# Performance work log

Hardware: AMD Instinct MI355X
Metric: run time of the kernel (lower is better)

## Reference

```python
import jax, jax.numpy as jnp
import numpy as np

B, D, HID, DC, K = 32768, 64, 512, 128, 12
CLAMP = 1.0
L1 = D // 2          # GLOW split lengths
L2 = D - L1
INIT = 0.01          # torch code rescales all params to 0.01*randn


def setup_inputs() -> dict:
    key = jax.random.key(0)
    ks = iter(jax.random.split(key, 16))
    # FrEIA PermuteRandom: np.random.seed(k); np.random.permutation(D)
    perms = jnp.asarray(
        np.stack([np.random.RandomState(k).permutation(D) for k in range(K)]),
        dtype=jnp.int32)
    f32 = jnp.float32
    return {
        'q_feat': jax.random.normal(next(ks), (B, 1, D), f32),
        'H': jax.random.normal(next(ks), (B, DC), f32),
        'perms': perms,
        'an_logscale': INIT * jax.random.normal(next(ks), (K, D), f32),
        'an_bias': INIT * jax.random.normal(next(ks), (K, D), f32),
        's1_W1': INIT * jax.random.normal(next(ks), (K, HID, L1 + DC), f32),
        's1_b1': INIT * jax.random.normal(next(ks), (K, HID), f32),
        's1_W2': INIT * jax.random.normal(next(ks), (K, 2 * L2, HID), f32),
        's1_b2': INIT * jax.random.normal(next(ks), (K, 2 * L2), f32),
        's2_W1': INIT * jax.random.normal(next(ks), (K, HID, L2 + DC), f32),
        's2_b1': INIT * jax.random.normal(next(ks), (K, HID), f32),
        's2_W2': INIT * jax.random.normal(next(ks), (K, 2 * L1, HID), f32),
        's2_b2': INIT * jax.random.normal(next(ks), (K, 2 * L1), f32),
    }


def _mlp(x, W1, b1, W2, b2):
    # torch Linear: y = x @ W.T + b
    h = jax.nn.relu(x @ W1.T + b1)
    return h @ W2.T + b2


def _log_e(s):
    # FrEIA GLOW soft clamp: log e(s) = clamp * 0.636 * atan(s / clamp)
    return CLAMP * 0.636 * jnp.arctan(s / CLAMP)


def reference(q_feat, H, perms, an_logscale, an_bias,
              s1_W1, s1_b1, s1_W2, s1_b2,
              s2_W1, s2_b1, s2_W2, s2_b2):
    x = q_feat.reshape(q_feat.shape[0], -1)          # Flatten: (B,1,D)->(B,D)
    logj = jnp.zeros(x.shape[0], x.dtype)

    def block(carry, p):
        x, logj = carry
        perm, ls, bi, w11, b11, w12, b12, w21, b21, w22, b22 = p
        x = x[:, perm]                               # PermuteRandom (logdet 0)
        x = x * jnp.exp(ls) + bi                     # ActNorm
        logj = logj + jnp.sum(ls)
        x1, x2 = x[:, :L1], x[:, L1:]                # GLOW coupling
        r2 = _mlp(jnp.concatenate([x2, H], 1), w21, b21, w22, b22)
        le2 = _log_e(r2[:, :L1])
        y1 = jnp.exp(le2) * x1 + r2[:, L1:]
        r1 = _mlp(jnp.concatenate([y1, H], 1), w11, b11, w12, b12)
        le1 = _log_e(r1[:, :L2])
        y2 = jnp.exp(le1) * x2 + r1[:, L2:]
        logj = logj + jnp.sum(le1, axis=1) + jnp.sum(le2, axis=1)
        return (jnp.concatenate([y1, y2], 1), logj), None

    (z, logj), _ = jax.lax.scan(
        block, (x, logj),
        (perms, an_logscale, an_bias,
         s1_W1, s1_b1, s1_W2, s1_b2,
         s2_W1, s2_b1, s2_W2, s2_b2))
    return z, logj
```

## Files before the change

kernel.cpp:

```cpp
#include <hip/hip_runtime.h>
#include <hip/hip_bf16.h>
#include <math.h>

#define B_ROWS 32768

typedef __attribute__((ext_vector_type(8)))  short        s8v;
typedef __attribute__((ext_vector_type(4)))  float        f4v;
typedef __attribute__((ext_vector_type(2)))  unsigned int u2v;
typedef __attribute__((ext_vector_type(4)))  unsigned int u4v;

__device__ __forceinline__ short f2bf(float f){
  unsigned u = __builtin_bit_cast(unsigned, f);
  u = (u + 0x7fffu + ((u >> 16) & 1u)) >> 16;
  return (short)u;
}
__device__ __forceinline__ unsigned pk2(float a, float b){
  return (unsigned)(unsigned short)f2bf(a) | ((unsigned)(unsigned short)f2bf(b) << 16);
}
__device__ __forceinline__ float bf_lo(unsigned u){ return __builtin_bit_cast(float, u << 16); }
__device__ __forceinline__ float bf_hi(unsigned u){ return __builtin_bit_cast(float, u & 0xffff0000u); }

#define MFMA16(A,B,C) __builtin_amdgcn_mfma_f32_16x16x32_bf16((A),(B),(C),0,0,0)

#define OXFT 0
#define XFT_S 132
#define OHB  33792
#define HB_S 136
#define OW1  68608
#define W1BUF 43008
#define W1_S 168
#define OB1  154624
#define OB2  158720
#define OLJ  159232
#define OPERM 159744
#define OELS 160000
#define OBIV 160256
#define OSLS 160512
#define SM_SZ 160528

#define SL_S 68
#define SLOT_B 17408

#define O_S1W1 0
#define O_S1W2 983040
#define O_S2W1 1376256
#define O_S2W2 2359296
#define W_TOTAL 2752512

__global__ void cvtw(const float* __restrict__ s1w1, const float* __restrict__ s1w2,
                     const float* __restrict__ s2w1, const float* __restrict__ s2w2,
                     unsigned short* __restrict__ dst)
{
  long t = (long)blockIdx.x * blockDim.x + threadIdx.x;
  if (t >= W_TOTAL) return;
  float v;
  if      (t < O_S1W2) v = s1w1[t];
  else if (t < O_S2W1) v = s1w2[t - O_S1W2];
  else if (t < O_S2W2) v = s2w1[t - O_S2W1];
  else                 v = s2w2[t - O_S2W2];
  dst[t] = (unsigned short)f2bf(v);
}

template<int USEBF>
__device__ __forceinline__ s8v ldw(const unsigned short* wb, const float* wf, int off){
  if (USEBF){
    return *(const s8v*)(wb + off);
  } else {
    f4v a = *(const f4v*)(wf + off);
    f4v b = *(const f4v*)(wf + off + 4);
    s8v r;
    r[0]=f2bf(a[0]); r[1]=f2bf(a[1]); r[2]=f2bf(a[2]); r[3]=f2bf(a[3]);
    r[4]=f2bf(b[0]); r[5]=f2bf(b[1]); r[6]=f2bf(b[2]); r[7]=f2bf(b[3]);
    return r;
  }
}

struct MP { const unsigned short* w1b; const float* w1f;
            const unsigned short* w2b; const float* w2f;
            const float* b1; const float* b2; };

__device__ __forceinline__ MP getmp(int m, const unsigned short* wbf,
    const float* s1W1f, const float* s1W2f, const float* s2W1f, const float* s2W2f,
    const float* s1b1, const float* s1b2, const float* s2b1, const float* s2b2)
{
  int blk = m >> 1;
  MP r;
  if (m & 1){
    r.w1b = wbf + O_S1W1 + (size_t)blk*81920; r.w1f = s1W1f + (size_t)blk*81920;
    r.w2b = wbf + O_S1W2 + (size_t)blk*32768; r.w2f = s1W2f + (size_t)blk*32768;
    r.b1 = s1b1 + blk*512; r.b2 = s1b2 + blk*64;
  } else {
    r.w1b = wbf + O_S2W1 + (size_t)blk*81920; r.w1f = s2W1f + (size_t)blk*81920;
    r.w2b = wbf + O_S2W2 + (size_t)blk*32768; r.w2f = s2W2f + (size_t)blk*32768;
    r.b1 = s2b1 + blk*512; r.b2 = s2b2 + blk*64;
  }
  return r;
}

template<int USEBF>
__device__ __forceinline__ void issue_w1(const MP& p, int cchunk, int tid,
                                         u4v wt[5], f4v wtf[10])
{
  if (USEBF){
    const unsigned short* s = p.w1b + cchunk*20480;
    #pragma unroll
    for (int k = 0; k < 5; ++k) wt[k] = *(const u4v*)(s + (size_t)(k*512+tid)*8);
  } else {
    const float* s = p.w1f + cchunk*20480;
    #pragma unroll
    for (int k = 0; k < 10; ++k) wtf[k] = *(const f4v*)(s + (size_t)(k*512+tid)*4);
  }
}

template<int USEBF>
__device__ __forceinline__ void write_w1(char* sm, int buf, int tid,
                                         const u4v wt[5], const f4v wtf[10])
{
  short* W1n = (short*)(sm + OW1 + buf*W1BUF);
  if (USEBF){
    #pragma unroll
    for (int k = 0; k < 5; ++k){
      int i = k*512 + tid, row = i/20, c16 = i - row*20;
      *(u4v*)(W1n + row*W1_S + c16*8) = wt[k];
    }
  } else {
    #pragma unroll
    for (int k = 0; k < 10; ++k){
      int i = k*512 + tid, row = i/40, c4 = i - row*40;
      f4v v = wtf[k];
      *(u2v*)(W1n + row*W1_S + c4*4) = (u2v){pk2(v[0],v[1]), pk2(v[2],v[3])};
    }
  }
}

template<int USEBF>
__device__ __forceinline__ void load_w2(const MP& p, int c, int hw, int l15, int lq, s8v w2o[4]){
  #pragma unroll
  for (int ot = 0; ot < 4; ++ot)
    w2o[ot] = ldw<USEBF>(p.w2b, p.w2f, (ot*16 + l15)*512 + c*128 + hw*32 + lq*8);
}

template<int USEBF>
__device__ __forceinline__ void mlp_body(char* sm, int tid, int m,
    const MP& cur, const MP& nxt, const s8v hfr[4][4], s8v w2cur[4])
{
  const int lane = tid & 63, wave = tid >> 6;
  const int hw = wave >> 1, ng = wave & 1;
  const int l15 = lane & 15, lq = lane >> 4;
  const int bp = m & 1;
  float* XFT = (float*)(sm + OXFT);
  short* HB  = (short*)(sm + OHB);
  float* B1L = (float*)(sm + OB1);
  float* B2L = (float*)(sm + OB2);
  float* LOGJ= (float*)(sm + OLJ);

  const int xbase = bp ? 0 : 32;
  s8v xk[4];
  #pragma unroll
  for (int nt = 0; nt < 4; ++nt){
    int b = ng*64 + nt*16 + l15;
    s8v v;
    #pragma unroll
    for (int i = 0; i < 8; ++i)
      v[i] = f2bf(XFT[(xbase + lq*8 + i)*XFT_S + b]);
    xk[nt] = v;
  }

  f4v racc[4][4];
  #pragma unroll
  for (int ot = 0; ot < 4; ++ot){
    f4v bv = (f4v){0.f,0.f,0.f,0.f};
    if (hw == 0) bv = *(const f4v*)(B2L + bp*64 + ot*16 + lq*4);
    #pragma unroll
    for (int nt = 0; nt < 4; ++nt) racc[ot][nt] = bv;
  }

  #pragma unroll
  for (int c = 0; c < 4; ++c){
    u4v wt[5]; f4v wtf[10];
    const MP& pn = (c < 3) ? cur : nxt;
    const int cn = (c < 3) ? c + 1 : 0;
    issue_w1<USEBF>(pn, cn, tid, wt, wtf);
    float b1t = 0.f, b2t = 0.f;
    if (c == 3){
      b1t = nxt.b1[tid];
      if (tid < 64) b2t = nxt.b2[tid];
    }

    const short* W1c = (const short*)(sm + OW1 + (c&1)*W1BUF);
    f4v acc[2][4];
    #pragma unroll
    for (int mt = 0; mt < 2; ++mt){
      f4v bv = *(const f4v*)(B1L + bp*512 + c*128 + hw*32 + mt*16 + lq*4);
      #pragma unroll
      for (int nt = 0; nt < 4; ++nt) acc[mt][nt] = bv;
    }
    #pragma unroll
    for (int kk = 0; kk < 5; ++kk){
      s8v a0 = *(const s8v*)(W1c + (hw*32 +  0 + l15)*W1_S + kk*32 + lq*8);
      s8v a1 = *(const s8v*)(W1c + (hw*32 + 16 + l15)*W1_S + kk*32 + lq*8);
      #pragma unroll
      for (int nt = 0; nt < 4; ++nt){
        s8v bb = (kk == 0) ? xk[nt] : hfr[nt][kk-1];
        acc[0][nt] = MFMA16(a0, bb, acc[0][nt]);
        acc[1][nt] = MFMA16(a1, bb, acc[1][nt]);
      }
    }
    #pragma unroll
    for (int mt = 0; mt < 2; ++mt)
      #pragma unroll
      for (int nt = 0; nt < 4; ++nt){
        float h0 = fmaxf(acc[mt][nt][0],0.f), h1 = fmaxf(acc[mt][nt][1],0.f);
        float h2 = fmaxf(acc[mt][nt][2],0.f), h3 = fmaxf(acc[mt][nt][3],0.f);
        *(u2v*)(HB + (ng*64 + nt*16 + l15)*HB_S + hw*32 + mt*16 + lq*4) = (u2v){pk2(h0,h1), pk2(h2,h3)};
      }
    #pragma unroll
    for (int nt = 0; nt < 4; ++nt){
      s8v bb = *(const s8v*)(HB + (ng*64 + nt*16 + l15)*HB_S + hw*32 + lq*8);
      #pragma unroll
      for (int ot = 0; ot < 4; ++ot)
        racc[ot][nt] = MFMA16(w2cur[ot], bb, racc[ot][nt]);
    }
    write_w1<USEBF>(sm, cn & 1, tid, wt, wtf);
    if (c == 3){
      B1L[(bp^1)*512 + tid] = b1t;
      if (tid < 64) B2L[(bp^1)*64 + tid] = b2t;
    }
    load_w2<USEBF>(pn, cn, hw, l15, lq, w2cur);
    __syncthreads();
  }

  {
    short* SL = (hw < 2) ? (short*)(sm + OW1 + W1BUF + hw*SLOT_B)
                         : (short*)(sm + OHB + (hw-2)*SLOT_B);
    #pragma unroll
    for (int ot = 0; ot < 4; ++ot)
      #pragma unroll
      for (int nt = 0; nt < 4; ++nt)
        *(u2v*)(SL + (ng*64 + nt*16 + l15)*SL_S + ot*16 + lq*4) =
          (u2v){pk2(racc[ot][nt][0], racc[ot][nt][1]), pk2(racc[ot][nt][2], racc[ot][nt][3])};
  }
  __syncthreads();

  {
    int b = tid & 127, og = tid >> 7;
    float le[8] = {0,0,0,0,0,0,0,0}, ra[8] = {0,0,0,0,0,0,0,0};
    #pragma unroll
    for (int mslot = 0; mslot < 4; ++mslot){
      const short* SL = (mslot < 2) ? (const short*)(sm + OW1 + W1BUF + mslot*SLOT_B)
                                    : (const short*)(sm + OHB + (mslot-2)*SLOT_B);
      u2v L0 = *(const u2v*)(SL + b*SL_S + og*8);
      u2v L1 = *(const u2v*)(SL + b*SL_S + og*8 + 4);
      u2v R0 = *(const u2v*)(SL + b*SL_S + 32 + og*8);
      u2v R1 = *(const u2v*)(SL + b*SL_S + 32 + og*8 + 4);
      le[0]+=bf_lo(L0[0]); le[1]+=bf_hi(L0[0]); le[2]+=bf_lo(L0[1]); le[3]+=bf_hi(L0[1]);
      le[4]+=bf_lo(L1[0]); le[5]+=bf_hi(L1[0]); le[6]+=bf_lo(L1[1]); le[7]+=bf_hi(L1[1]);
      ra[0]+=bf_lo(R0[0]); ra[1]+=bf_hi(R0[0]); ra[2]+=bf_lo(R0[1]); ra[3]+=bf_hi(R0[1]);
      ra[4]+=bf_lo(R1[0]); ra[5]+=bf_hi(R1[0]); ra[6]+=bf_lo(R1[1]); ra[7]+=bf_hi(R1[1]);
    }
    float part = 0.f;
    #pragma unroll
    for (int j = 0; j < 8; ++j){
      float l = 0.636f * atanf(le[j]);
      int d = bp*32 + og*8 + j;
      float y = __expf(l) * XFT[d*XFT_S + b] + ra[j];
      XFT[d*XFT_S + b] = y;
      part += l;
    }
    atomicAdd(&LOGJ[b], part);
  }
  __syncthreads();
}

template<int USEBF>
__global__ __launch_bounds__(512, 2) void cinn_t(
    const float* __restrict__ q, const float* __restrict__ Hg,
    const int* __restrict__ perms,
    const float* __restrict__ ls_g, const float* __restrict__ bi_g,
    const float* __restrict__ s1b1, const float* __restrict__ s1b2,
    const float* __restrict__ s2b1, const float* __restrict__ s2b2,
    const unsigned short* __restrict__ wbf,
    const float* __restrict__ s1W1f, const float* __restrict__ s1W2f,
    const float* __restrict__ s2W1f, const float* __restrict__ s2W2f,
    float* __restrict__ outz, float* __restrict__ outlj)
{
  __shared__ __align__(16) char sm[SM_SZ];
  const int tid = threadIdx.x;
  const int rowbase = blockIdx.x * 128;
  const int lane = tid & 63, wave = tid >> 6;
  const int hw = wave >> 1, ng = wave & 1;
  const int l15 = lane & 15, lq = lane >> 4;

  float* XFT = (float*)(sm + OXFT);
  float* B1L = (float*)(sm + OB1);
  float* B2L = (float*)(sm + OB2);
  float* LOGJ = (float*)(sm + OLJ);
  int*   PERM = (int*)(sm + OPERM);
  float* ELS  = (float*)(sm + OELS);
  float* BIV  = (float*)(sm + OBIV);
  float* SLSp = (float*)(sm + OSLS);

  {
    int b = tid >> 2, j = tid & 3;
    const float* src = q + (size_t)(rowbase + b)*64 + j*16;
    #pragma unroll
    for (int i = 0; i < 4; ++i){
      f4v v = *(const f4v*)(src + 4*i);
      #pragma unroll
      for (int jj = 0; jj < 4; ++jj)
        XFT[(j*16 + 4*i + jj)*XFT_S + b] = v[jj];
    }
  }
  if (tid < 128) LOGJ[tid] = 0.f;
  if (tid == 0)  *SLSp = 0.f;
  __syncthreads();
  if (tid < 64){
    float p = 0.f;
    #pragma unroll
    for (int k = 0; k < 12; ++k) p += ls_g[k*64 + tid];
    atomicAdd(SLSp, p);
  }

  s8v hfr[4][4];
  #pragma unroll
  for (int nt = 0; nt < 4; ++nt){
    int b = rowbase + ng*64 + nt*16 + l15;
    #pragma unroll
    for (int kkh = 0; kkh < 4; ++kkh){
      const float* hp = Hg + (size_t)b*128 + kkh*32 + lq*8;
      f4v a = *(const f4v*)hp;
      f4v c = *(const f4v*)(hp + 4);
      s8v r;
      r[0]=f2bf(a[0]); r[1]=f2bf(a[1]); r[2]=f2bf(a[2]); r[3]=f2bf(a[3]);
      r[4]=f2bf(c[0]); r[5]=f2bf(c[1]); r[6]=f2bf(c[2]); r[7]=f2bf(c[3]);
      hfr[nt][kkh] = r;
    }
  }

  s8v w2cur[4];
  {
    MP p0 = getmp(0, wbf, s1W1f, s1W2f, s2W1f, s2W2f, s1b1, s1b2, s2b1, s2b2);
    u4v wt[5]; f4v wtf[10];
    issue_w1<USEBF>(p0, 0, tid, wt, wtf);
    write_w1<USEBF>(sm, 0, tid, wt, wtf);
    B1L[tid] = p0.b1[tid];
    if (tid < 64) B2L[tid] = p0.b2[tid];
    load_w2<USEBF>(p0, 0, hw, l15, lq, w2cur);
  }

  for (int m = 0; m < 24; ++m){
    if (!(m & 1)){
      int blk = m >> 1;
      if (tid < 64){
        PERM[tid] = perms[blk*64 + tid];
        ELS[tid]  = __expf(ls_g[blk*64 + tid]);
        BIV[tid]  = bi_g[blk*64 + tid];
      }
      __syncthreads();
      {
        int d = lane, bg = wave;
        int pd = PERM[d];
        f4v v[4];
        #pragma unroll
        for (int i = 0; i < 4; ++i)
          v[i] = *(const f4v*)(XFT + pd*XFT_S + bg*16 + 4*i);
        __syncthreads();
        float e = ELS[d], bi = BIV[d];
        #pragma unroll
        for (int i = 0; i < 4; ++i){
          #pragma unroll
          for (int jj = 0; jj < 4; ++jj) v[i][jj] = fmaf(v[i][jj], e, bi);
          *(f4v*)(XFT + d*XFT_S + bg*16 + 4*i) = v[i];
        }
      }
      __syncthreads();
    }
    MP cur = getmp(m, wbf, s1W1f, s1W2f, s2W1f, s2W2f, s1b1, s1b2, s2b1, s2b2);
    MP nxt = getmp(m < 23 ? m + 1 : 23, wbf, s1W1f, s1W2f, s2W1f, s2W2f, s1b1, s1b2, s2b1, s2b2);
    mlp_body<USEBF>(sm, tid, m, cur, nxt, hfr, w2cur);
  }

  {
    int b = tid >> 2, j = tid & 3;
    float* dst = outz + (size_t)(rowbase + b)*64 + j*16;
    #pragma unroll
    for (int i = 0; i < 4; ++i){
      f4v w;
      #pragma unroll
      for (int jj = 0; jj < 4; ++jj)
        w[jj] = XFT[(j*16 + 4*i + jj)*XFT_S + b];
      *(f4v*)(dst + 4*i) = w;
    }
  }
  if (tid < 128) outlj[rowbase + tid] = LOGJ[tid] + *SLSp;
}

extern "C" void kernel_launch(void* const* d_in, const int* in_sizes, int n_in,
                              void* d_out, int out_size, void* d_ws, size_t ws_size,
                              hipStream_t stream)
{
  const float* q    = (const float*)d_in[0];
  const float* Hg   = (const float*)d_in[1];
  const int*   perms= (const int*)  d_in[2];
  const float* ls   = (const float*)d_in[3];
  const float* bi   = (const float*)d_in[4];
  const float* s1W1 = (const float*)d_in[5];
  const float* s1b1 = (const float*)d_in[6];
  const float* s1W2 = (const float*)d_in[7];
  const float* s1b2 = (const float*)d_in[8];
  const float* s2W1 = (const float*)d_in[9];
  const float* s2b1 = (const float*)d_in[10];
  const float* s2W2 = (const float*)d_in[11];
  const float* s2b2 = (const float*)d_in[12];
  float* outz  = (float*)d_out;
  float* outlj = outz + (size_t)B_ROWS * 64;

  int usebf = (ws_size >= (size_t)W_TOTAL * 2) ? 1 : 0;
  unsigned short* wbf = (unsigned short*)d_ws;
  if (usebf){
    cvtw<<<2688, 1024, 0, stream>>>(s1W1, s1W2, s2W1, s2W2, wbf);
    cinn_t<1><<<256, 512, 0, stream>>>(q, Hg, perms, ls, bi,
                                       s1b1, s1b2, s2b1, s2b2,
                                       wbf, s1W1, s1W2, s2W1, s2W2,
                                       outz, outlj);
  } else {
    cinn_t<0><<<256, 512, 0, stream>>>(q, Hg, perms, ls, bi,
                                       s1b1, s1b2, s2b1, s2b2,
                                       wbf, s1W1, s1W2, s2W1, s2W2,
                                       outz, outlj);
  }
}
```

Before: 299.2 us.

## Keep biases in registers, precompute W1 store indices, use hardware bf16 packing

Biases for both MLP layers now live in per-thread registers, loaded from global memory one chunk ahead, so the shared-memory bias buffers and their stores are removed. The per-thread row and column indices for the W1 staging stores are computed once instead of being recomputed by integer division every chunk. Float-to-bf16 conversion switches to the library __float2bfloat16 with paired packing. Launch bounds drop from 2 blocks per CU to 1, which frees registers for the extra state but may cost occupancy.

```diff
diff --git a/kernel.cpp b/kernel.cpp
--- a/kernel.cpp
+++ b/kernel.cpp
@@ -14,8 +14,10 @@
   u = (u + 0x7fffu + ((u >> 16) & 1u)) >> 16;
   return (short)u;
 }
-__device__ __forceinline__ unsigned pk2(float a, float b){
-  return (unsigned)(unsigned short)f2bf(a) | ((unsigned)(unsigned short)f2bf(b) << 16);
+__device__ __forceinline__ unsigned cpk(float a, float b){
+  __hip_bfloat16_raw lo = (__hip_bfloat16_raw)__float2bfloat16(a);
+  __hip_bfloat16_raw hi = (__hip_bfloat16_raw)__float2bfloat16(b);
+  return (unsigned)lo.x | ((unsigned)hi.x << 16);
 }
 __device__ __forceinline__ float bf_lo(unsigned u){ return __builtin_bit_cast(float, u << 16); }
 __device__ __forceinline__ float bf_hi(unsigned u){ return __builtin_bit_cast(float, u & 0xffff0000u); }
@@ -29,17 +31,16 @@
 #define OW1  68608
 #define W1BUF 43008
 #define W1_S 168
-#define OB1  154624
-#define OB2  158720
-#define OLJ  159232
-#define OPERM 159744
-#define OELS 160000
-#define OBIV 160256
-#define OSLS 160512
-#define SM_SZ 160528
+#define OLJ  154624
+#define OPERM 155136
+#define OELS 155392
+#define OBIV 155648
+#define OSLS 155904
+#define SM_SZ 155920
 
 #define SL_S 68
 #define SLOT_B 17408
+#define OSL0 (OW1 + W1BUF)
 
 #define O_S1W1 0
 #define O_S1W2 983040
@@ -68,10 +69,8 @@
   } else {
     f4v a = *(const f4v*)(wf + off);
     f4v b = *(const f4v*)(wf + off + 4);
-    s8v r;
-    r[0]=f2bf(a[0]); r[1]=f2bf(a[1]); r[2]=f2bf(a[2]); r[3]=f2bf(a[3]);
-    r[4]=f2bf(b[0]); r[5]=f2bf(b[1]); r[6]=f2bf(b[2]); r[7]=f2bf(b[3]);
-    return r;
+    u4v u = {cpk(a[0],a[1]), cpk(a[2],a[3]), cpk(b[0],b[1]), cpk(b[2],b[3])};
+    return __builtin_bit_cast(s8v, u);
   }
 }
 
@@ -113,22 +112,20 @@
 }
 
 template<int USEBF>
-__device__ __forceinline__ void write_w1(char* sm, int buf, int tid,
-                                         const u4v wt[5], const f4v wtf[10])
+__device__ __forceinline__ void write_w1(char* sm, int buf,
+                                         const u4v wt[5], const f4v wtf[10],
+                                         const int* wr, const int* wc)
 {
   short* W1n = (short*)(sm + OW1 + buf*W1BUF);
   if (USEBF){
     #pragma unroll
-    for (int k = 0; k < 5; ++k){
-      int i = k*512 + tid, row = i/20, c16 = i - row*20;
-      *(u4v*)(W1n + row*W1_S + c16*8) = wt[k];
-    }
+    for (int k = 0; k < 5; ++k)
+      *(u4v*)(W1n + wr[k]*W1_S + wc[k]*8) = wt[k];
   } else {
     #pragma unroll
     for (int k = 0; k < 10; ++k){
-      int i = k*512 + tid, row = i/40, c4 = i - row*40;
       f4v v = wtf[k];
-      *(u2v*)(W1n + row*W1_S + c4*4) = (u2v){pk2(v[0],v[1]), pk2(v[2],v[3])};
+      *(u2v*)(W1n + wr[k]*W1_S + wc[k]*4) = (u2v){cpk(v[0],v[1]), cpk(v[2],v[3])};
     }
   }
 }
@@ -142,7 +139,8 @@
 
 template<int USEBF>
 __device__ __forceinline__ void mlp_body(char* sm, int tid, int m,
-    const MP& cur, const MP& nxt, const s8v hfr[4][4], s8v w2cur[4])
+    const MP& cur, const MP& nxt, const s8v hfr[4][4], s8v w2cur[4],
+    f4v b1cur[2], f4v b2cur[4], const int* wr, const int* wc)
 {
   const int lane = tid & 63, wave = tid >> 6;
   const int hw = wave >> 1, ng = wave & 1;
@@ -150,8 +148,6 @@
   const int bp = m & 1;
   float* XFT = (float*)(sm + OXFT);
   short* HB  = (short*)(sm + OHB);
-  float* B1L = (float*)(sm + OB1);
-  float* B2L = (float*)(sm + OB2);
   float* LOGJ= (float*)(sm + OLJ);
 
   const int xbase = bp ? 0 : 32;
@@ -159,18 +155,19 @@
   #pragma unroll
   for (int nt = 0; nt < 4; ++nt){
     int b = ng*64 + nt*16 + l15;
-    s8v v;
-    #pragma unroll
-    for (int i = 0; i < 8; ++i)
-      v[i] = f2bf(XFT[(xbase + lq*8 + i)*XFT_S + b]);
-    xk[nt] = v;
+    const float* xp = XFT + (xbase + lq*8)*XFT_S + b;
+    u4v u;
+    #pragma unroll
+    for (int p = 0; p < 4; ++p)
+      u[p] = cpk(xp[(2*p)*XFT_S], xp[(2*p+1)*XFT_S]);
+    xk[nt] = __builtin_bit_cast(s8v, u);
   }
 
   f4v racc[4][4];
   #pragma unroll
   for (int ot = 0; ot < 4; ++ot){
     f4v bv = (f4v){0.f,0.f,0.f,0.f};
-    if (hw == 0) bv = *(const f4v*)(B2L + bp*64 + ot*16 + lq*4);
+    if (hw == 0) bv = b2cur[ot];
     #pragma unroll
     for (int nt = 0; nt < 4; ++nt) racc[ot][nt] = bv;
   }
@@ -181,17 +178,19 @@
     const MP& pn = (c < 3) ? cur : nxt;
     const int cn = (c < 3) ? c + 1 : 0;
     issue_w1<USEBF>(pn, cn, tid, wt, wtf);
-    float b1t = 0.f, b2t = 0.f;
-    if (c == 3){
-      b1t = nxt.b1[tid];
-      if (tid < 64) b2t = nxt.b2[tid];
+    f4v b1n0 = *(const f4v*)(pn.b1 + cn*128 + hw*32 + lq*4);
+    f4v b1n1 = *(const f4v*)(pn.b1 + cn*128 + hw*32 + 16 + lq*4);
+    if (c == 3 && hw == 0){
+      #pragma unroll
+      for (int ot = 0; ot < 4; ++ot)
+        b2cur[ot] = *(const f4v*)(nxt.b2 + ot*16 + lq*4);
     }
 
     const short* W1c = (const short*)(sm + OW1 + (c&1)*W1BUF);
     f4v acc[2][4];
     #pragma unroll
     for (int mt = 0; mt < 2; ++mt){
-      f4v bv = *(const f4v*)(B1L + bp*512 + c*128 + hw*32 + mt*16 + lq*4);
+      f4v bv = b1cur[mt];
       #pragma unroll
       for (int nt = 0; nt < 4; ++nt) acc[mt][nt] = bv;
     }
@@ -212,7 +211,7 @@
       for (int nt = 0; nt < 4; ++nt){
         float h0 = fmaxf(acc[mt][nt][0],0.f), h1 = fmaxf(acc[mt][nt][1],0.f);
         float h2 = fmaxf(acc[mt][nt][2],0.f), h3 = fmaxf(acc[mt][nt][3],0.f);
-        *(u2v*)(HB + (ng*64 + nt*16 + l15)*HB_S + hw*32 + mt*16 + lq*4) = (u2v){pk2(h0,h1), pk2(h2,h3)};
+        *(u2v*)(HB + (ng*64 + nt*16 + l15)*HB_S + hw*32 + mt*16 + lq*4) = (u2v){cpk(h0,h1), cpk(h2,h3)};
       }
     #pragma unroll
     for (int nt = 0; nt < 4; ++nt){
@@ -221,24 +220,21 @@
       for (int ot = 0; ot < 4; ++ot)
         racc[ot][nt] = MFMA16(w2cur[ot], bb, racc[ot][nt]);
     }
-    write_w1<USEBF>(sm, cn & 1, tid, wt, wtf);
-    if (c == 3){
-      B1L[(bp^1)*512 + tid] = b1t;
-      if (tid < 64) B2L[(bp^1)*64 + tid] = b2t;
-    }
+    write_w1<USEBF>(sm, cn & 1, wt, wtf, wr, wc);
+    b1cur[0] = b1n0; b1cur[1] = b1n1;
     load_w2<USEBF>(pn, cn, hw, l15, lq, w2cur);
     __syncthreads();
   }
 
   {
-    short* SL = (hw < 2) ? (short*)(sm + OW1 + W1BUF + hw*SLOT_B)
+    short* SL = (hw < 2) ? (short*)(sm + OSL0 + hw*SLOT_B)
                          : (short*)(sm + OHB + (hw-2)*SLOT_B);
     #pragma unroll
     for (int ot = 0; ot < 4; ++ot)
       #pragma unroll
       for (int nt = 0; nt < 4; ++nt)
         *(u2v*)(SL + (ng*64 + nt*16 + l15)*SL_S + ot*16 + lq*4) =
-          (u2v){pk2(racc[ot][nt][0], racc[ot][nt][1]), pk2(racc[ot][nt][2], racc[ot][nt][3])};
+          (u2v){cpk(racc[ot][nt][0], racc[ot][nt][1]), cpk(racc[ot][nt][2], racc[ot][nt][3])};
   }
   __syncthreads();
 
@@ -247,7 +243,7 @@
     float le[8] = {0,0,0,0,0,0,0,0}, ra[8] = {0,0,0,0,0,0,0,0};
     #pragma unroll
     for (int mslot = 0; mslot < 4; ++mslot){
-      const short* SL = (mslot < 2) ? (const short*)(sm + OW1 + W1BUF + mslot*SLOT_B)
+      const short* SL = (mslot < 2) ? (const short*)(sm + OSL0 + mslot*SLOT_B)
                                     : (const short*)(sm + OHB + (mslot-2)*SLOT_B);
       u2v L0 = *(const u2v*)(SL + b*SL_S + og*8);
       u2v L1 = *(const u2v*)(SL + b*SL_S + og*8 + 4);
@@ -273,7 +269,7 @@
 }
 
 template<int USEBF>
-__global__ __launch_bounds__(512, 2) void cinn_t(
+__global__ __launch_bounds__(512, 1) void cinn_t(
     const float* __restrict__ q, const float* __restrict__ Hg,
     const int* __restrict__ perms,
     const float* __restrict__ ls_g, const float* __restrict__ bi_g,
@@ -292,14 +288,21 @@
   const int l15 = lane & 15, lq = lane >> 4;
 
   float* XFT = (float*)(sm + OXFT);
-  float* B1L = (float*)(sm + OB1);
-  float* B2L = (float*)(sm + OB2);
   float* LOGJ = (float*)(sm + OLJ);
   int*   PERM = (int*)(sm + OPERM);
   float* ELS  = (float*)(sm + OELS);
   float* BIV  = (float*)(sm + OBIV);
   float* SLSp = (float*)(sm + OSLS);
 
+  int wr[10], wc[10];
+  if (USEBF){
+    #pragma unroll
+    for (int k = 0; k < 5; ++k){ int i = k*512 + tid; wr[k] = i/20; wc[k] = i - wr[k]*20; }
+  } else {
+    #pragma unroll
+    for (int k = 0; k < 10; ++k){ int i = k*512 + tid; wr[k] = i/40; wc[k] = i - wr[k]*40; }
+  }
+
   {
     int b = tid >> 2, j = tid & 3;
     const float* src = q + (size_t)(rowbase + b)*64 + j*16;
@@ -330,21 +333,25 @@
       const float* hp = Hg + (size_t)b*128 + kkh*32 + lq*8;
       f4v a = *(const f4v*)hp;
       f4v c = *(const f4v*)(hp + 4);
-      s8v r;
-      r[0]=f2bf(a[0]); r[1]=f2bf(a[1]); r[2]=f2bf(a[2]); r[3]=f2bf(a[3]);
-      r[4]=f2bf(c[0]); r[5]=f2bf(c[1]); r[6]=f2bf(c[2]); r[7]=f2bf(c[3]);
-      hfr[nt][kkh] = r;
+      u4v u = {cpk(a[0],a[1]), cpk(a[2],a[3]), cpk(c[0],c[1]), cpk(c[2],c[3])};
+      hfr[nt][kkh] = __builtin_bit_cast(s8v, u);
     }
   }
 
   s8v w2cur[4];
+  f4v b1cur[2], b2cur[4];
   {
     MP p0 = getmp(0, wbf, s1W1f, s1W2f, s2W1f, s2W2f, s1b1, s1b2, s2b1, s2b2);
     u4v wt[5]; f4v wtf[10];
     issue_w1<USEBF>(p0, 0, tid, wt, wtf);
-    write_w1<USEBF>(sm, 0, tid, wt, wtf);
-    B1L[tid] = p0.b1[tid];
-    if (tid < 64) B2L[tid] = p0.b2[tid];
+    write_w1<USEBF>(sm, 0, wt, wtf, wr, wc);
+    b1cur[0] = *(const f4v*)(p0.b1 + hw*32 + lq*4);
+    b1cur[1] = *(const f4v*)(p0.b1 + hw*32 + 16 + lq*4);
+    if (hw == 0){
+      #pragma unroll
+      for (int ot = 0; ot < 4; ++ot)
+        b2cur[ot] = *(const f4v*)(p0.b2 + ot*16 + lq*4);
+    }
     load_w2<USEBF>(p0, 0, hw, l15, lq, w2cur);
   }
 
@@ -377,7 +384,7 @@
     }
     MP cur = getmp(m, wbf, s1W1f, s1W2f, s2W1f, s2W2f, s1b1, s1b2, s2b1, s2b2);
     MP nxt = getmp(m < 23 ? m + 1 : 23, wbf, s1W1f, s1W2f, s2W1f, s2W2f, s1b1, s1b2, s2b1, s2b2);
-    mlp_body<USEBF>(sm, tid, m, cur, nxt, hfr, w2cur);
+    mlp_body<USEBF>(sm, tid, m, cur, nxt, hfr, w2cur, b1cur, b2cur, wr, wc);
   }
 
   {
```

Measured after the change: 308.7 us. +3.2%, slower.
